# Kernel optimization log

Hardware: AMD Instinct MI355X
Metric: run time of the kernel (lower is better)

The kernel has to match this reference:

```python
import jax, jax.numpy as jnp
import numpy as np

B, S, D_MODEL = 2, 2048, 2048
NUM_HEADS, NUM_KV_HEADS, HEAD_DIM = 16, 4, 128
MAX_SEQ = 2048
ROPE_WAVELENGTH = 10000.0


def apply_rope(x, positions, head_dim, max_wavelength):
    # x: [B, S, H, D], positions: [B, S]
    fraction = 2.0 * jnp.arange(0, head_dim // 2, dtype=jnp.float32) / head_dim
    timescale = max_wavelength ** fraction                      # [D/2]
    sinusoid = positions[..., None].astype(jnp.float32) / timescale  # [B,S,D/2]
    sin = jnp.sin(sinusoid)[:, :, None, :]                      # [B,S,1,D/2]
    cos = jnp.cos(sinusoid)[:, :, None, :]
    x1, x2 = jnp.split(x, 2, axis=-1)
    first = x1 * cos - x2 * sin
    second = x2 * cos + x1 * sin
    return jnp.concatenate([first, second], axis=-1).astype(x.dtype)


def setup_inputs() -> dict:
    key = jax.random.key(0)
    ks = jax.random.split(key, 5)
    inputs = jax.random.normal(ks[0], (B, S, D_MODEL), dtype=jnp.float32)
    seq_pos = jnp.broadcast_to(jnp.arange(S, dtype=jnp.int32)[None, :], (B, S))
    std = 0.01  # nnx.initializers.normal() default stddev
    wq = jax.random.normal(ks[1], (D_MODEL, NUM_HEADS, HEAD_DIM), dtype=jnp.float32) * std
    bq = jnp.zeros((NUM_HEADS, HEAD_DIM), dtype=jnp.float32)
    wkv = jax.random.normal(ks[2], (D_MODEL, NUM_KV_HEADS, 2 * HEAD_DIM), dtype=jnp.float32) * std
    bkv = jnp.zeros((NUM_KV_HEADS, 2 * HEAD_DIM), dtype=jnp.float32)
    wo = jax.random.normal(ks[3], (NUM_HEADS, HEAD_DIM, D_MODEL), dtype=jnp.float32) * std
    bo = jnp.zeros((D_MODEL,), dtype=jnp.float32)
    return {"inputs": inputs, "seq_pos": seq_pos, "wq": wq, "bq": bq,
            "wkv": wkv, "bkv": bkv, "wo": wo, "bo": bo}


def reference(inputs, seq_pos, wq, bq, wkv, bkv, wo, bo):
    dtype = inputs.dtype
    # Projections
    kv = jnp.einsum('bsd,dkh->bskh', inputs, wkv) + bkv          # [B,S,KV,2*HD]
    key, value = jnp.split(kv, 2, axis=-1)                       # [B,S,KV,HD] each
    query = jnp.einsum('bsd,dnh->bsnh', inputs, wq) + bq         # [B,S,H,HD]
    # RoPE
    query = apply_rope(query, seq_pos, HEAD_DIM, ROPE_WAVELENGTH)
    key = apply_rope(key, seq_pos, HEAD_DIM, ROPE_WAVELENGTH)
    # GQA: repeat KV heads
    rep = NUM_HEADS // NUM_KV_HEADS
    key_r = jnp.repeat(key, rep, axis=2)                          # [B,S,H,HD]
    value_r = jnp.repeat(value, rep, axis=2)
    # Attention (einsum_attention path)
    q = query / jnp.sqrt(jnp.asarray(HEAD_DIM, dtype=dtype))
    attn = jnp.einsum('bqhd,bkhd->bhqk', q, key_r)               # [B,H,S,S]
    # position_mask: seq_range <= time_steps -> causal
    seq_range = jnp.arange(MAX_SEQ, dtype=jnp.int32)
    mask = (seq_range[None, None, :] <= seq_pos[:, :, None])[:, None, :, :]  # [B,1,S,S]
    big_neg = jnp.finfo(dtype).min
    attn = jnp.where(mask, attn, big_neg)
    attn = jax.nn.softmax(attn, axis=-1).astype(dtype)
    x = jnp.einsum('bhqk,bkhd->bqhd', attn, value_r)             # [B,S,H,HD]
    out = jnp.einsum('bqhd,hdo->bqo', x, wo) + bo                # [B,S,D]
    return out
```

## Files before the change

### kernel.cpp

```cpp
#include <hip/hip_runtime.h>
#include <hip/hip_bf16.h>

#define DM    2048
#define SEQ   2048
#define NB    2
#define NH    16
#define NKVH  4
#define HD    128
#define NQKV  3072
#define MROWS 4096
#define KVB   64
#define QSC   0.08838834764831845f

using f32x4  = __attribute__((ext_vector_type(4))) float;
using short8 = __attribute__((ext_vector_type(8))) short;
using ushort8 = __attribute__((ext_vector_type(8))) unsigned short;

static __device__ __forceinline__ unsigned short f2bf(float f) {
  __hip_bfloat16 h = __float2bfloat16(f);
  return *reinterpret_cast<unsigned short*>(&h);
}
static __device__ __forceinline__ float bf2f(unsigned short u) {
  union { unsigned int i; float f; } v; v.i = ((unsigned int)u) << 16; return v.f;
}

typedef __attribute__((address_space(1))) const unsigned char as1_c;
typedef __attribute__((address_space(3))) unsigned char as3_c;
static __device__ __forceinline__ void gload_lds16(const void* g, void* l) {
  __builtin_amdgcn_global_load_lds((as1_c*)g, (as3_c*)l, 16, 0, 0);
}


__global__ void build_trig(float2* __restrict__ tbl) {
  int i = blockIdx.x * 256 + threadIdx.x;
  int p = i >> 6, d = i & 63;
  float inv_ts = powf(10000.0f, -(float)d * (1.0f / 64.0f));
  float ang = (float)p * inv_ts;
  float sn, cs;
  sincosf(ang, &sn, &cs);
  tbl[i] = make_float2(cs, sn);
}


__global__ void f32_to_bf16_vec(const float* __restrict__ src, unsigned short* __restrict__ dst, int n4) {
  int i = blockIdx.x * blockDim.x + threadIdx.x;
  if (i < n4) {
    float4 v = reinterpret_cast<const float4*>(src)[i];
    ushort4 o;
    o.x = f2bf(v.x); o.y = f2bf(v.y); o.z = f2bf(v.z); o.w = f2bf(v.w);
    reinterpret_cast<ushort4*>(dst)[i] = o;
  }
}

__global__ void transpose_all(const float* __restrict__ wq, const float* __restrict__ wkv,
                              const float* __restrict__ wo,
                              unsigned short* __restrict__ WqkvT, unsigned short* __restrict__ WoT) {
  int bx = blockIdx.x;
  const float* src; unsigned short* dst; int N;
  if (bx < 64)       { src = wq;  dst = WqkvT;                         N = 2048; }
  else if (bx < 96)  { src = wkv; dst = WqkvT + (size_t)2048 * DM;     N = 1024; bx -= 64; }
  else               { src = wo;  dst = WoT;                           N = 2048; bx -= 96; }
  __shared__ float t[32][33];
  int n0 = bx * 32, k0 = blockIdx.y * 32;
  int tx = threadIdx.x, ty = threadIdx.y;
  for (int j = 0; j < 4; j++)
    t[ty + j * 8][tx] = src[(size_t)(k0 + ty + j * 8) * N + n0 + tx];
  __syncthreads();
  for (int j = 0; j < 4; j++)
    dst[(size_t)(n0 + ty + j * 8) * DM + k0 + tx] = f2bf(t[tx][ty + j * 8]);
}

__global__ void bias_concat(const float* __restrict__ bq, const float* __restrict__ bkv, float* __restrict__ o) {
  int i = blockIdx.x * 256 + threadIdx.x;
  if (i < NQKV) o[i] = (i < DM) ? bq[i] : bkv[i - DM];
}


#define STA(buf, kt, q) gload_lds16(gA + (size_t)((q) * 32) * K + (kt), LW + (buf) * 65536 + ((q) * 32 + rowA) * 128)
#define STB(buf, kt, h) gload_lds16(gB + (size_t)((h) * 64) * K + (kt), LW + (buf) * 65536 + 32768 + ((h) * 64 + rowB) * 128)

#define RDB(buf) \
  _Pragma("unroll") for (int ni = 0; ni < 4; ++ni) { \
    int row_ = (EPI == 1) ? (wc * 16 + ni * 64 + ln) : (wc * 64 + ni * 16 + ln); \
    const char* p_ = (const char*)LW + (buf) * 65536 + 32768 + row_ * 128; \
    bfr[ni][0] = *(const short8*)(p_ + coff0); \
    bfr[ni][1] = *(const short8*)(p_ + coff1); }

#define RDA(buf, q) \
  _Pragma("unroll") for (int m2 = 0; m2 < 2; ++m2) { \
    int row_ = wr * 128 + ((q) * 2 + m2) * 16 + ln; \
    const char* p_ = (const char*)LW + (buf) * 65536 + row_ * 128; \
    af[m2][0] = *(const short8*)(p_ + coff0); \
    af[m2][1] = *(const short8*)(p_ + coff1); }

#define MFQ(q) \
  _Pragma("unroll") for (int m2 = 0; m2 < 2; ++m2) \
  _Pragma("unroll") for (int ni = 0; ni < 4; ++ni) { \
    acc[(q) * 2 + m2][ni] = __builtin_amdgcn_mfma_f32_16x16x32_bf16(af[m2][0], bfr[ni][0], acc[(q) * 2 + m2][ni], 0, 0, 0); \
    acc[(q) * 2 + m2][ni] = __builtin_amdgcn_mfma_f32_16x16x32_bf16(af[m2][1], bfr[ni][1], acc[(q) * 2 + m2][ni], 0, 0, 0); }

#define SYNC_IN() do { __builtin_amdgcn_sched_barrier(0); __builtin_amdgcn_s_barrier(); \
  asm volatile("s_waitcnt lgkmcnt(0)" ::: "memory"); __builtin_amdgcn_sched_barrier(0); \
  __builtin_amdgcn_s_setprio(1); } while (0)
#define SYNC_OUT() do { __builtin_amdgcn_s_setprio(0); __builtin_amdgcn_sched_barrier(0); \
  __builtin_amdgcn_s_barrier(); } while (0)
#define SYNC_OUT_VM() do { __builtin_amdgcn_s_setprio(0); \
  asm volatile("s_waitcnt vmcnt(6)" ::: "memory"); __builtin_amdgcn_sched_barrier(0); \
  __builtin_amdgcn_s_barrier(); } while (0)

template <int EPI>
__global__ __launch_bounds__(512, 2) void gemm8(
    const unsigned short* __restrict__ A, const unsigned short* __restrict__ Bt,
    const float* __restrict__ bias, const int* __restrict__ seq_pos,
    const float2* __restrict__ tbl,
    unsigned short* __restrict__ Qo, unsigned short* __restrict__ Ko,
    unsigned short* __restrict__ Vo, float* __restrict__ Cout,
    int nbx, int N, int K) {
  __shared__ __align__(16) unsigned short lds[2 * 2 * 16384];
  int tid = threadIdx.x, lane = tid & 63, w = tid >> 6;
  int wr = w >> 2, wc = w & 3;
  int lg = lane >> 4, ln = lane & 15;

  int bid = blockIdx.x;
  int cpx = gridDim.x >> 3;
  int swz = (bid & 7) * cpx + (bid >> 3);
  int by = swz / nbx, bx = swz - by * nbx;
  int m0 = by * 256, n0 = bx * 256;

  int soff = ((lane & 7) ^ (lane >> 3)) << 3;
  const unsigned short* gA = A + (size_t)(m0 + ((w & 3) << 3) + ((w >> 2) << 7) + (lane >> 3)) * K + soff;
  const unsigned short* gB = Bt + (size_t)(n0 + (w << 3) + (lane >> 3)) * K + soff;
  char* LW = (char*)lds;
  int rowA = ((w & 3) << 3) + ((w >> 2) << 7);
  int rowB = (w << 3);
  int coff0 = ((lg)     ^ (ln & 7)) << 4;
  int coff1 = ((lg + 4) ^ (ln & 7)) << 4;

  f32x4 acc[8][4];
#pragma unroll
  for (int mi = 0; mi < 8; ++mi)
#pragma unroll
    for (int ni = 0; ni < 4; ++ni) acc[mi][ni] = (f32x4){0, 0, 0, 0};

  short8 bfr[4][2], af[2][2];

  STB(0, 0, 0); STB(0, 0, 1); STB(0, 0, 2); STB(0, 0, 3);
  STA(0, 0, 0); STA(0, 0, 1); STA(0, 0, 2); STA(0, 0, 3);
  STB(1, 64, 0); STB(1, 64, 1); STB(1, 64, 2); STB(1, 64, 3);
  STA(1, 64, 0); STA(1, 64, 1);
  asm volatile("s_waitcnt vmcnt(6)" ::: "memory");
  __builtin_amdgcn_sched_barrier(0);
  __builtin_amdgcn_s_barrier();

  for (int it = 0; it < (K >> 7); ++it) {
    int kt1  = it * 128 + 64;
    int ktn0 = (it * 128 + 128) & (K - 1);
    int ktn1 = (it * 128 + 192) & (K - 1);
    RDB(0); RDA(0, 0);
    STA(1, kt1, 2); STA(1, kt1, 3);
    SYNC_IN(); MFQ(0); SYNC_OUT();
    RDA(0, 1);
    STB(0, ktn0, 0); STB(0, ktn0, 1);
    SYNC_IN(); MFQ(1); SYNC_OUT();
    RDA(0, 2);
    STB(0, ktn0, 2); STB(0, ktn0, 3);
    SYNC_IN(); MFQ(2); SYNC_OUT();
    RDA(0, 3);
    STA(0, ktn0, 0); STA(0, ktn0, 1);
    SYNC_IN(); MFQ(3); SYNC_OUT_VM();
    RDB(1); RDA(1, 0);
    STA(0, ktn0, 2); STA(0, ktn0, 3);
    SYNC_IN(); MFQ(0); SYNC_OUT();
    RDA(1, 1);
    STB(1, ktn1, 0); STB(1, ktn1, 1);
    SYNC_IN(); MFQ(1); SYNC_OUT();
    RDA(1, 2);
    STB(1, ktn1, 2); STB(1, ktn1, 3);
    SYNC_IN(); MFQ(2); SYNC_OUT();
    RDA(1, 3);
    STA(1, ktn1, 0); STA(1, ktn1, 1);
    SYNC_IN(); MFQ(3); SYNC_OUT_VM();
  }
  asm volatile("s_waitcnt vmcnt(0)" ::: "memory");

  if constexpr (EPI == 0) {
#pragma unroll
    for (int mi = 0; mi < 8; ++mi) {
      int row = m0 + wr * 128 + mi * 16 + lg * 4;
#pragma unroll
      for (int ni = 0; ni < 4; ++ni) {
        int col = n0 + wc * 64 + ni * 16 + ln;
        float bv = bias[col];
#pragma unroll
        for (int r = 0; r < 4; ++r)
          Cout[(size_t)(row + r) * N + col] = acc[mi][ni][r] + bv;
      }
    }
  } else {
    int d = wc * 16 + ln;
    float bv0 = bias[n0 + d],      bv1 = bias[n0 + d + 64];
    float bv2 = bias[n0 + d + 128], bv3 = bias[n0 + d + 192];
    int bI = m0 >> 11, s0 = m0 & (SEQ - 1);
    int nt = n0 >> 8;
    if (nt < 8) {
      unsigned short* qp0 = Qo + (size_t)(bI * NH + nt * 2) * SEQ * HD;
      unsigned short* qp1 = qp0 + (size_t)SEQ * HD;
#pragma unroll
      for (int mi = 0; mi < 8; ++mi) {
        int sl = wr * 128 + mi * 16 + lg * 4;
#pragma unroll
        for (int r = 0; r < 4; ++r) {
          int s = s0 + sl + r;
          int pos = seq_pos[bI * SEQ + s];
          float2 cs = tbl[pos * 64 + d];
          float x1 = acc[mi][0][r] + bv0, x2 = acc[mi][1][r] + bv1;
          float y1 = acc[mi][2][r] + bv2, y2 = acc[mi][3][r] + bv3;
          unsigned short* q0 = qp0 + (size_t)s * HD;
          q0[d]      = f2bf((x1 * cs.x - x2 * cs.y) * QSC);
          q0[d + 64] = f2bf((x2 * cs.x + x1 * cs.y) * QSC);
          unsigned short* q1 = qp1 + (size_t)s * HD;
          q1[d]      = f2bf((y1 * cs.x - y2 * cs.y) * QSC);
          q1[d + 64] = f2bf((y2 * cs.x + y1 * cs.y) * QSC);
        }
      }
    } else {
      int kvh = nt - 8;
      unsigned short* kp = Ko + (size_t)(bI * NKVH + kvh) * SEQ * HD;
      unsigned short* vp = Vo + (size_t)(bI * NKVH + kvh) * HD * SEQ;
#pragma unroll
      for (int mi = 0; mi < 8; ++mi) {
        int sl = wr * 128 + mi * 16 + lg * 4;
        ushort4 v0q, v1q;
#pragma unroll
        for (int r = 0; r < 4; ++r) {
          int s = s0 + sl + r;
          int pos = seq_pos[bI * SEQ + s];
          float2 cs = tbl[pos * 64 + d];
          float x1 = acc[mi][0][r] + bv0, x2 = acc[mi][1][r] + bv1;
          unsigned short* krow = kp + (size_t)s * HD;
          krow[d]      = f2bf(x1 * cs.x - x2 * cs.y);
          krow[d + 64] = f2bf(x2 * cs.x + x1 * cs.y);
          ((unsigned short*)&v0q)[r] = f2bf(acc[mi][2][r] + bv2);
          ((unsigned short*)&v1q)[r] = f2bf(acc[mi][3][r] + bv3);
        }
        *(ushort4*)(vp + (size_t)d * SEQ + s0 + sl)        = v0q;
        *(ushort4*)(vp + (size_t)(d + 64) * SEQ + s0 + sl) = v1q;
      }
    }
  }
}


__global__ __launch_bounds__(256) void flash_attn(const unsigned short* __restrict__ Q,
                                                  const unsigned short* __restrict__ Kr,
                                                  const unsigned short* __restrict__ Vt,
                                                  const int* __restrict__ seq_pos,
                                                  unsigned short* __restrict__ X) {
  __shared__ __align__(16) unsigned short lds_k[64 * 128];
  __shared__ __align__(16) unsigned short lds_v[128 * 64];
  __shared__ __align__(16) unsigned short lds_p[4][16 * 64];
  int tid = threadIdx.x, lane = tid & 63, w = tid >> 6;
  int bh = blockIdx.y, b = bh >> 4, h = bh & 15, kvh = h >> 2;
  int lg = lane >> 4, ln = lane & 15;

  const unsigned short* kbase = Kr + ((size_t)(b * NKVH + kvh)) * SEQ * HD;
  const unsigned short* vbase = Vt + ((size_t)(b * NKVH + kvh)) * HD * SEQ;

  const unsigned short* gks[4]; unsigned short* lks[4];
  const unsigned short* gvs[4]; unsigned short* lvs[4];
#pragma unroll
  for (int i = 0; i < 4; i++) {
    int kr = w * 16 + i * 4 + (lane >> 4);
    int kc = (lane & 15) ^ (kr & 7);
    gks[i] = kbase + (size_t)kr * HD + kc * 8;
    lks[i] = lds_k + (w * 16 + i * 4) * 128;
    int vr = w * 32 + i * 8 + (lane >> 3);
    int vc = (lane & 7) ^ (vr & 7);
    gvs[i] = vbase + (size_t)vr * SEQ + vc * 8;
    lvs[i] = lds_v + (w * 32 + i * 8) * 64;
  }

  const short8 ones = {0x3F80, 0x3F80, 0x3F80, 0x3F80, 0x3F80, 0x3F80, 0x3F80, 0x3F80};

  for (int pass = 0; pass < 2; pass++) {
    int qtile = (pass == 0) ? (int)blockIdx.x : (SEQ / 64 - 1 - (int)blockIdx.x);
    int qblk = qtile * 64;
    int q0w = qblk + w * 16;

    int pmax = seq_pos[b * SEQ + qblk + lane];
    for (int o = 32; o; o >>= 1) { int t2 = __shfl_xor(pmax, o); pmax = pmax > t2 ? pmax : t2; }
    int ntiles = (pmax + KVB) >> 6;
    if (ntiles > SEQ / KVB) ntiles = SEQ / KVB;

    int pos_r[4];
    for (int r = 0; r < 4; r++) pos_r[r] = seq_pos[b * SEQ + q0w + lg * 4 + r];

    short8 qf[4];
    {
      const unsigned short* qp = Q + ((size_t)((b * NH + h) * SEQ + q0w + ln)) * HD;
      for (int c = 0; c < 4; c++) qf[c] = *reinterpret_cast<const short8*>(qp + c * 32 + lg * 8);
    }

    f32x4 acc[8];
    for (int dt = 0; dt < 8; dt++) acc[dt] = (f32x4){0, 0, 0, 0};
    f32x4 lacc = (f32x4){0, 0, 0, 0};
    float m_r[4] = {-1e30f, -1e30f, -1e30f, -1e30f};

    for (int t = 0; t < ntiles; t++) {
      int kv0 = t * KVB;
#pragma unroll
      for (int i = 0; i < 4; i++) {
        gload_lds16(gks[i] + (size_t)kv0 * HD, lks[i]);
        gload_lds16(gvs[i] + kv0, lvs[i]);
      }
      __syncthreads();

      f32x4 sa[4];
#pragma unroll
      for (int ct = 0; ct < 4; ct++) {
        sa[ct] = (f32x4){0, 0, 0, 0};
        int row = ct * 16 + ln;
        const char* kr0 = (const char*)lds_k + row * 256;
        int sw = (row & 7) << 4;
#pragma unroll
        for (int c = 0; c < 4; c++) {
          short8 kf = *reinterpret_cast<const short8*>(kr0 + ((c * 64 + lg * 16) ^ sw));
          sa[ct] = __builtin_amdgcn_mfma_f32_16x16x32_bf16(qf[c], kf, sa[ct], 0, 0, 0);
        }
      }

      float p[4][4], corr[4];
#pragma unroll
      for (int r = 0; r < 4; r++) {
        int kv = kv0 + ln;
        float v0 = (kv      <= pos_r[r]) ? sa[0][r] : -1e30f;
        float v1 = (kv + 16 <= pos_r[r]) ? sa[1][r] : -1e30f;
        float v2 = (kv + 32 <= pos_r[r]) ? sa[2][r] : -1e30f;
        float v3 = (kv + 48 <= pos_r[r]) ? sa[3][r] : -1e30f;
        float tmx = fmaxf(fmaxf(v0, v1), fmaxf(v2, v3));
        tmx = fmaxf(tmx, __shfl_xor(tmx, 1));
        tmx = fmaxf(tmx, __shfl_xor(tmx, 2));
        tmx = fmaxf(tmx, __shfl_xor(tmx, 4));
        tmx = fmaxf(tmx, __shfl_xor(tmx, 8));
        float nm = fmaxf(m_r[r], tmx);
        corr[r] = __expf(m_r[r] - nm);
        p[0][r] = __expf(v0 - nm); p[1][r] = __expf(v1 - nm);
        p[2][r] = __expf(v2 - nm); p[3][r] = __expf(v3 - nm);
        m_r[r] = nm;
      }

      {
        char* pw = (char*)lds_p[w];
#pragma unroll
        for (int r = 0; r < 4; r++) {
          int row = lg * 4 + r;
          int sw2 = (row & 7) << 4;
          char* pr = pw + row * 128;
#pragma unroll
          for (int ct = 0; ct < 4; ct++)
            *reinterpret_cast<unsigned short*>(pr + (((ct * 16 + ln) * 2) ^ sw2)) = f2bf(p[ct][r]);
        }
      }

#pragma unroll
      for (int dt = 0; dt < 8; dt++)
#pragma unroll
        for (int r = 0; r < 4; r++) acc[dt][r] *= corr[r];
#pragma unroll
      for (int r = 0; r < 4; r++) lacc[r] *= corr[r];

      asm volatile("s_waitcnt lgkmcnt(0)" ::: "memory");
      __builtin_amdgcn_sched_barrier(0);
      short8 pf[2];
      {
        const char* pr = (const char*)lds_p[w] + ln * 128;
        int sw2 = (ln & 7) << 4;
        pf[0] = *reinterpret_cast<const short8*>(pr + ((lg * 16) ^ sw2));
        pf[1] = *reinterpret_cast<const short8*>(pr + ((64 + lg * 16) ^ sw2));
      }

#pragma unroll
      for (int dt = 0; dt < 8; dt++) {
        int row = dt * 16 + ln;
        const char* vr0 = (const char*)lds_v + row * 128;
        int sw3 = (row & 7) << 4;
        short8 vf0 = *reinterpret_cast<const short8*>(vr0 + ((lg * 16) ^ sw3));
        short8 vf1 = *reinterpret_cast<const short8*>(vr0 + ((64 + lg * 16) ^ sw3));
        acc[dt] = __builtin_amdgcn_mfma_f32_16x16x32_bf16(pf[0], vf0, acc[dt], 0, 0, 0);
        acc[dt] = __builtin_amdgcn_mfma_f32_16x16x32_bf16(pf[1], vf1, acc[dt], 0, 0, 0);
      }
      lacc = __builtin_amdgcn_mfma_f32_16x16x32_bf16(pf[0], ones, lacc, 0, 0, 0);
      lacc = __builtin_amdgcn_mfma_f32_16x16x32_bf16(pf[1], ones, lacc, 0, 0, 0);
      __syncthreads();
    }

    for (int r = 0; r < 4; r++) {
      float inv = lacc[r] > 0.0f ? 1.0f / lacc[r] : 0.0f;
      int qrow = q0w + lg * 4 + r;
      unsigned short* xp = X + ((size_t)(b * SEQ + qrow)) * DM + h * HD;
      for (int dt = 0; dt < 8; dt++) xp[dt * 16 + ln] = f2bf(acc[dt][r] * inv);
    }
  }
}


extern "C" void kernel_launch(void* const* d_in, const int* in_sizes, int n_in,
                              void* d_out, int out_size, void* d_ws, size_t ws_size,
                              hipStream_t stream) {
  const float* inputs  = (const float*)d_in[0];
  const int*   seq_pos = (const int*)d_in[1];
  const float* wq  = (const float*)d_in[2];
  const float* bq  = (const float*)d_in[3];
  const float* wkv = (const float*)d_in[4];
  const float* bkv = (const float*)d_in[5];
  const float* wo  = (const float*)d_in[6];
  const float* bo  = (const float*)d_in[7];
  float* out = (float*)d_out;

  char* ws = (char*)d_ws;
  unsigned short* Abf     = (unsigned short*)(ws + 0);
  unsigned short* WqkvT   = (unsigned short*)(ws + 16777216);
  unsigned short* WoT     = (unsigned short*)(ws + 29360128);
  float*          biasqkv = (float*)(ws + 37748736);
  float2*         tbl     = (float2*)(ws + 37761024);
  unsigned short* Qr      = (unsigned short*)(ws + 38809600);
  unsigned short* Kr      = (unsigned short*)(ws + 55586816);
  unsigned short* Vt      = (unsigned short*)(ws + 59781120);
  unsigned short* Xb      = (unsigned short*)(ws + 63975424);

  build_trig<<<512, 256, 0, stream>>>(tbl);
  f32_to_bf16_vec<<<8192, 256, 0, stream>>>(inputs, Abf, (NB * SEQ * DM) / 4);
  transpose_all<<<dim3(160, 64), dim3(32, 8), 0, stream>>>(wq, wkv, wo, WqkvT, WoT);
  bias_concat<<<12, 256, 0, stream>>>(bq, bkv, biasqkv);

  gemm8<1><<<(MROWS / 256) * (NQKV / 256), 512, 0, stream>>>(
      Abf, WqkvT, biasqkv, seq_pos, tbl, Qr, Kr, Vt, nullptr, NQKV / 256, NQKV, DM);

  flash_attn<<<dim3(SEQ / 128, NB * NH), 256, 0, stream>>>(Qr, Kr, Vt, seq_pos, Xb);

  gemm8<0><<<(MROWS / 256) * (DM / 256), 512, 0, stream>>>(
      Xb, WoT, bo, nullptr, nullptr, nullptr, nullptr, nullptr, out, DM / 256, DM, DM);
}
```

Baseline: 314.6 us.

## Rewrite flash attention with 32x32 MFMA, register-resident P and lazy rescaling

The attention kernel moves from 16x16x32 MFMA tiles with P staged through LDS to 32x32x16 MFMA tiles computing S^T, so each lane owns one query row. P is converted to bf16 in registers with packed converts and a permlane32 swap, which removes the LDS round trip and the ones-MFMA row sum. The kernel also adds a threshold-based skip of the running-max rescale, masks only on diagonal tiles, and sets MFMA priority hints. Each block now handles one 128-row query tile in reverse order instead of two paired 64-row tiles, which loses the previous causal load balancing and may raise register pressure.

```diff
diff --git a/kernel.cpp b/kernel.cpp
--- a/kernel.cpp
+++ b/kernel.cpp
@@ -13,8 +13,10 @@
 #define QSC   0.08838834764831845f
 
 using f32x4  = __attribute__((ext_vector_type(4))) float;
+using f32x16 = __attribute__((ext_vector_type(16))) float;
 using short8 = __attribute__((ext_vector_type(8))) short;
 using ushort8 = __attribute__((ext_vector_type(8))) unsigned short;
+using uint2v = __attribute__((ext_vector_type(2))) unsigned int;
 
 static __device__ __forceinline__ unsigned short f2bf(float f) {
   __hip_bfloat16 h = __float2bfloat16(f);
@@ -22,6 +24,11 @@
 }
 static __device__ __forceinline__ float bf2f(unsigned short u) {
   union { unsigned int i; float f; } v; v.i = ((unsigned int)u) << 16; return v.f;
+}
+static __device__ __forceinline__ unsigned cvtpk_bf16(float lo, float hi) {
+  unsigned r;
+  asm("v_cvt_pk_bf16_f32 %0, %1, %2" : "=v"(r) : "v"(lo), "v"(hi));
+  return r;
 }
 
 typedef __attribute__((address_space(1))) const unsigned char as1_c;
@@ -251,20 +258,22 @@
 }
 
 
-__global__ __launch_bounds__(256) void flash_attn(const unsigned short* __restrict__ Q,
-                                                  const unsigned short* __restrict__ Kr,
-                                                  const unsigned short* __restrict__ Vt,
-                                                  const int* __restrict__ seq_pos,
-                                                  unsigned short* __restrict__ X) {
+__global__ __launch_bounds__(256, 2) void flash_attn(const unsigned short* __restrict__ Q,
+                                                     const unsigned short* __restrict__ Kr,
+                                                     const unsigned short* __restrict__ Vt,
+                                                     const int* __restrict__ seq_pos,
+                                                     unsigned short* __restrict__ X) {
   __shared__ __align__(16) unsigned short lds_k[64 * 128];
   __shared__ __align__(16) unsigned short lds_v[128 * 64];
-  __shared__ __align__(16) unsigned short lds_p[4][16 * 64];
   int tid = threadIdx.x, lane = tid & 63, w = tid >> 6;
-  int bh = blockIdx.y, b = bh >> 4, h = bh & 15, kvh = h >> 2;
-  int lg = lane >> 4, ln = lane & 15;
-
-  const unsigned short* kbase = Kr + ((size_t)(b * NKVH + kvh)) * SEQ * HD;
-  const unsigned short* vbase = Vt + ((size_t)(b * NKVH + kvh)) * HD * SEQ;
+  int hi = lane >> 5, q5 = lane & 31;
+  int bh = blockIdx.y, b = bh >> 4, h = bh & 15, kvhh = h >> 2;
+  int qtile = 15 - (int)blockIdx.x;
+  int qbase = qtile * 128;
+  int q_global = qbase + w * 32 + q5;
+
+  const unsigned short* kbase = Kr + ((size_t)(b * NKVH + kvhh)) * SEQ * HD;
+  const unsigned short* vbase = Vt + ((size_t)(b * NKVH + kvhh)) * HD * SEQ;
 
   const unsigned short* gks[4]; unsigned short* lks[4];
   const unsigned short* gvs[4]; unsigned short* lvs[4];
@@ -280,127 +289,144 @@
     lvs[i] = lds_v + (w * 32 + i * 8) * 64;
   }
 
-  const short8 ones = {0x3F80, 0x3F80, 0x3F80, 0x3F80, 0x3F80, 0x3F80, 0x3F80, 0x3F80};
-
-  for (int pass = 0; pass < 2; pass++) {
-    int qtile = (pass == 0) ? (int)blockIdx.x : (SEQ / 64 - 1 - (int)blockIdx.x);
-    int qblk = qtile * 64;
-    int q0w = qblk + w * 16;
-
-    int pmax = seq_pos[b * SEQ + qblk + lane];
-    for (int o = 32; o; o >>= 1) { int t2 = __shfl_xor(pmax, o); pmax = pmax > t2 ? pmax : t2; }
-    int ntiles = (pmax + KVB) >> 6;
-    if (ntiles > SEQ / KVB) ntiles = SEQ / KVB;
-
-    int pos_r[4];
-    for (int r = 0; r < 4; r++) pos_r[r] = seq_pos[b * SEQ + q0w + lg * 4 + r];
-
-    short8 qf[4];
-    {
-      const unsigned short* qp = Q + ((size_t)((b * NH + h) * SEQ + q0w + ln)) * HD;
-      for (int c = 0; c < 4; c++) qf[c] = *reinterpret_cast<const short8*>(qp + c * 32 + lg * 8);
-    }
-
-    f32x4 acc[8];
-    for (int dt = 0; dt < 8; dt++) acc[dt] = (f32x4){0, 0, 0, 0};
-    f32x4 lacc = (f32x4){0, 0, 0, 0};
-    float m_r[4] = {-1e30f, -1e30f, -1e30f, -1e30f};
-
-    for (int t = 0; t < ntiles; t++) {
-      int kv0 = t * KVB;
-#pragma unroll
-      for (int i = 0; i < 4; i++) {
-        gload_lds16(gks[i] + (size_t)kv0 * HD, lks[i]);
-        gload_lds16(gvs[i] + kv0, lvs[i]);
+  int pm = max(seq_pos[b * SEQ + qbase + lane], seq_pos[b * SEQ + qbase + 64 + lane]);
+#pragma unroll
+  for (int o = 32; o; o >>= 1) { int t2 = __shfl_xor(pm, o); pm = pm > t2 ? pm : t2; }
+  int ntiles = (pm + KVB) >> 6;
+  if (ntiles > SEQ / KVB) ntiles = SEQ / KVB;
+
+  int pos_q = seq_pos[b * SEQ + q_global];
+  int wmin = pos_q;
+#pragma unroll
+  for (int o = 32; o; o >>= 1) { int t2 = __shfl_xor(wmin, o); wmin = wmin < t2 ? wmin : t2; }
+
+  short8 qf[8];
+  {
+    const unsigned short* qp = Q + ((size_t)((b * NH + h) * SEQ + q_global)) * HD + hi * 8;
+#pragma unroll
+    for (int c = 0; c < 8; c++) qf[c] = *reinterpret_cast<const short8*>(qp + c * 16);
+  }
+
+  f32x16 acc[4];
+#pragma unroll
+  for (int db = 0; db < 4; db++)
+#pragma unroll
+    for (int r = 0; r < 16; ++r) acc[db][r] = 0.0f;
+  float m_q = -1e30f, l_q = 0.0f;
+
+  const char* kp0 = (const char*)lds_k + q5 * 256;
+  const char* kp1 = kp0 + 32 * 256;
+  int swk = (q5 & 7) << 4;
+
+  for (int t = 0; t < ntiles; t++) {
+    int kv0 = t * KVB;
+#pragma unroll
+    for (int i = 0; i < 4; i++) {
+      gload_lds16(gks[i] + (size_t)kv0 * HD, lks[i]);
+      gload_lds16(gvs[i] + kv0, lvs[i]);
+    }
+    __syncthreads();
+
+    f32x16 st0, st1;
+#pragma unroll
+    for (int r = 0; r < 16; ++r) { st0[r] = 0.0f; st1[r] = 0.0f; }
+    __builtin_amdgcn_s_setprio(1);
+#pragma unroll
+    for (int c = 0; c < 8; c++) {
+      short8 kf0 = *reinterpret_cast<const short8*>(kp0 + ((c * 32 + hi * 16) ^ swk));
+      short8 kf1 = *reinterpret_cast<const short8*>(kp1 + ((c * 32 + hi * 16) ^ swk));
+      st0 = __builtin_amdgcn_mfma_f32_32x32x16_bf16(kf0, qf[c], st0, 0, 0, 0);
+      st1 = __builtin_amdgcn_mfma_f32_32x32x16_bf16(kf1, qf[c], st1, 0, 0, 0);
+    }
+    __builtin_amdgcn_s_setprio(0);
+
+    if (kv0 + 63 > wmin) {
+      int kvb = kv0 + 4 * hi;
+#pragma unroll
+      for (int r = 0; r < 16; ++r) {
+        int kg = kvb + (r & 3) + 8 * (r >> 2);
+        if (kg > pos_q)      st0[r] = -1e30f;
+        if (kg + 32 > pos_q) st1[r] = -1e30f;
       }
-      __syncthreads();
-
-      f32x4 sa[4];
-#pragma unroll
-      for (int ct = 0; ct < 4; ct++) {
-        sa[ct] = (f32x4){0, 0, 0, 0};
-        int row = ct * 16 + ln;
-        const char* kr0 = (const char*)lds_k + row * 256;
-        int sw = (row & 7) << 4;
-#pragma unroll
-        for (int c = 0; c < 4; c++) {
-          short8 kf = *reinterpret_cast<const short8*>(kr0 + ((c * 64 + lg * 16) ^ sw));
-          sa[ct] = __builtin_amdgcn_mfma_f32_16x16x32_bf16(qf[c], kf, sa[ct], 0, 0, 0);
-        }
+    }
+
+    float tm[16];
+#pragma unroll
+    for (int r = 0; r < 16; ++r) tm[r] = fmaxf(st0[r], st1[r]);
+#pragma unroll
+    for (int s = 8; s; s >>= 1)
+#pragma unroll
+      for (int r = 0; r < s; ++r) tm[r] = fmaxf(tm[r], tm[r + s]);
+    float mx = fmaxf(tm[0], __shfl_xor(tm[0], 32));
+
+    bool skip = (mx <= m_q + 8.0f) && (m_q > -1e29f);
+    if (!__all((int)skip)) {
+      float nm = fmaxf(m_q, mx);
+      float corr = __expf(m_q - nm);
+      m_q = nm; l_q *= corr;
+#pragma unroll
+      for (int db = 0; db < 4; db++)
+#pragma unroll
+        for (int r = 0; r < 16; ++r) acc[db][r] *= corr;
+    }
+
+    float sm[16];
+#pragma unroll
+    for (int r = 0; r < 16; ++r) {
+      st0[r] = __expf(st0[r] - m_q);
+      st1[r] = __expf(st1[r] - m_q);
+      sm[r] = st0[r] + st1[r];
+    }
+#pragma unroll
+    for (int s = 8; s; s >>= 1)
+#pragma unroll
+      for (int r = 0; r < s; ++r) sm[r] += sm[r + s];
+    l_q += sm[0] + __shfl_xor(sm[0], 32);
+
+    short8 pb[4];
+#define MKFRAG(STV, B, OUT) { \
+    unsigned a_ = cvtpk_bf16(STV[(B) + 0], STV[(B) + 1]); \
+    unsigned b_ = cvtpk_bf16(STV[(B) + 2], STV[(B) + 3]); \
+    unsigned c_ = cvtpk_bf16(STV[(B) + 4], STV[(B) + 5]); \
+    unsigned d_ = cvtpk_bf16(STV[(B) + 6], STV[(B) + 7]); \
+    uint2v r1_ = __builtin_amdgcn_permlane32_swap(a_, c_, false, false); \
+    uint2v r2_ = __builtin_amdgcn_permlane32_swap(b_, d_, false, false); \
+    union { unsigned u[4]; short8 s; } f_; \
+    f_.u[0] = r1_[0]; f_.u[1] = r2_[0]; f_.u[2] = r1_[1]; f_.u[3] = r2_[1]; \
+    OUT = f_.s; }
+    MKFRAG(st0, 0, pb[0]);
+    MKFRAG(st0, 8, pb[1]);
+    MKFRAG(st1, 0, pb[2]);
+    MKFRAG(st1, 8, pb[3]);
+#undef MKFRAG
+
+    __builtin_amdgcn_s_setprio(1);
+#pragma unroll
+    for (int db = 0; db < 4; db++) {
+      const char* vr0 = (const char*)lds_v + (db * 32 + q5) * 128;
+#pragma unroll
+      for (int tt = 0; tt < 4; tt++) {
+        short8 vf = *reinterpret_cast<const short8*>(vr0 + ((tt * 32 + hi * 16) ^ swk));
+        acc[db] = __builtin_amdgcn_mfma_f32_32x32x16_bf16(vf, pb[tt], acc[db], 0, 0, 0);
       }
-
-      float p[4][4], corr[4];
-#pragma unroll
-      for (int r = 0; r < 4; r++) {
-        int kv = kv0 + ln;
-        float v0 = (kv      <= pos_r[r]) ? sa[0][r] : -1e30f;
-        float v1 = (kv + 16 <= pos_r[r]) ? sa[1][r] : -1e30f;
-        float v2 = (kv + 32 <= pos_r[r]) ? sa[2][r] : -1e30f;
-        float v3 = (kv + 48 <= pos_r[r]) ? sa[3][r] : -1e30f;
-        float tmx = fmaxf(fmaxf(v0, v1), fmaxf(v2, v3));
-        tmx = fmaxf(tmx, __shfl_xor(tmx, 1));
-        tmx = fmaxf(tmx, __shfl_xor(tmx, 2));
-        tmx = fmaxf(tmx, __shfl_xor(tmx, 4));
-        tmx = fmaxf(tmx, __shfl_xor(tmx, 8));
-        float nm = fmaxf(m_r[r], tmx);
-        corr[r] = __expf(m_r[r] - nm);
-        p[0][r] = __expf(v0 - nm); p[1][r] = __expf(v1 - nm);
-        p[2][r] = __expf(v2 - nm); p[3][r] = __expf(v3 - nm);
-        m_r[r] = nm;
-      }
-
-      {
-        char* pw = (char*)lds_p[w];
-#pragma unroll
-        for (int r = 0; r < 4; r++) {
-          int row = lg * 4 + r;
-          int sw2 = (row & 7) << 4;
-          char* pr = pw + row * 128;
-#pragma unroll
-          for (int ct = 0; ct < 4; ct++)
-            *reinterpret_cast<unsigned short*>(pr + (((ct * 16 + ln) * 2) ^ sw2)) = f2bf(p[ct][r]);
-        }
-      }
-
-#pragma unroll
-      for (int dt = 0; dt < 8; dt++)
-#pragma unroll
-        for (int r = 0; r < 4; r++) acc[dt][r] *= corr[r];
-#pragma unroll
-      for (int r = 0; r < 4; r++) lacc[r] *= corr[r];
-
-      asm volatile("s_waitcnt lgkmcnt(0)" ::: "memory");
-      __builtin_amdgcn_sched_barrier(0);
-      short8 pf[2];
-      {
-        const char* pr = (const char*)lds_p[w] + ln * 128;
-        int sw2 = (ln & 7) << 4;
-        pf[0] = *reinterpret_cast<const short8*>(pr + ((lg * 16) ^ sw2));
-        pf[1] = *reinterpret_cast<const short8*>(pr + ((64 + lg * 16) ^ sw2));
-      }
-
-#pragma unroll
-      for (int dt = 0; dt < 8; dt++) {
-        int row = dt * 16 + ln;
-        const char* vr0 = (const char*)lds_v + row * 128;
-        int sw3 = (row & 7) << 4;
-        short8 vf0 = *reinterpret_cast<const short8*>(vr0 + ((lg * 16) ^ sw3));
-        short8 vf1 = *reinterpret_cast<const short8*>(vr0 + ((64 + lg * 16) ^ sw3));
-        acc[dt] = __builtin_amdgcn_mfma_f32_16x16x32_bf16(pf[0], vf0, acc[dt], 0, 0, 0);
-        acc[dt] = __builtin_amdgcn_mfma_f32_16x16x32_bf16(pf[1], vf1, acc[dt], 0, 0, 0);
-      }
-      lacc = __builtin_amdgcn_mfma_f32_16x16x32_bf16(pf[0], ones, lacc, 0, 0, 0);
-      lacc = __builtin_amdgcn_mfma_f32_16x16x32_bf16(pf[1], ones, lacc, 0, 0, 0);
-      __syncthreads();
-    }
-
-    for (int r = 0; r < 4; r++) {
-      float inv = lacc[r] > 0.0f ? 1.0f / lacc[r] : 0.0f;
-      int qrow = q0w + lg * 4 + r;
-      unsigned short* xp = X + ((size_t)(b * SEQ + qrow)) * DM + h * HD;
-      for (int dt = 0; dt < 8; dt++) xp[dt * 16 + ln] = f2bf(acc[dt][r] * inv);
-    }
-  }
+    }
+    __builtin_amdgcn_s_setprio(0);
+    __syncthreads();
+  }
+
+  float inv = l_q > 0.0f ? 1.0f / l_q : 0.0f;
+  unsigned short* xp = X + ((size_t)(b * SEQ + q_global)) * DM + h * HD;
+#pragma unroll
+  for (int db = 0; db < 4; db++)
+#pragma unroll
+    for (int rq = 0; rq < 4; rq++) {
+      int d = db * 32 + 4 * hi + 8 * rq;
+      ushort4 o;
+      unsigned short* op = (unsigned short*)&o;
+#pragma unroll
+      for (int j = 0; j < 4; j++) op[j] = f2bf(acc[db][rq * 4 + j] * inv);
+      *(ushort4*)(xp + d) = o;
+    }
 }
 
 
@@ -436,7 +462,7 @@
   gemm8<1><<<(MROWS / 256) * (NQKV / 256), 512, 0, stream>>>(
       Abf, WqkvT, biasqkv, seq_pos, tbl, Qr, Kr, Vt, nullptr, NQKV / 256, NQKV, DM);
 
-  flash_attn<<<dim3(SEQ / 128, NB * NH), 256, 0, stream>>>(Qr, Kr, Vt, seq_pos, Xb);
+  flash_attn<<<dim3(16, NB * NH), 256, 0, stream>>>(Qr, Kr, Vt, seq_pos, Xb);
 
   gemm8<0><<<(MROWS / 256) * (DM / 256), 512, 0, stream>>>(
       Xb, WoT, bo, nullptr, nullptr, nullptr, nullptr, nullptr, out, DM / 256, DM, DM);
```

After: 308.8 us. About the same (-1.9%).
